# Performance work log

Measured on AMD Instinct MI355X. Metric: run time of the kernel, lower is better.

Reference implementation:

```python
import jax, jax.numpy as jnp
import numpy as np

D_MODEL = 1024
NUM_HEADS = 16
D_K = D_MODEL // NUM_HEADS
D_FF = 4096


def setup_inputs() -> dict:
    key = jax.random.key(0)
    ks = jax.random.split(key, 12)
    s = 1.0 / np.sqrt(D_MODEL)
    sf = 1.0 / np.sqrt(D_FF)
    return {
        "x": jax.random.normal(ks[0], (2, 2048, D_MODEL), dtype=jnp.float32),
        # nn.Linear weights are [out_features, in_features]
        "Wq": jax.random.uniform(ks[1], (D_MODEL, D_MODEL), jnp.float32, -s, s),
        "Wk": jax.random.uniform(ks[2], (D_MODEL, D_MODEL), jnp.float32, -s, s),
        "Wv": jax.random.uniform(ks[3], (D_MODEL, D_MODEL), jnp.float32, -s, s),
        "Wo": jax.random.uniform(ks[4], (D_MODEL, D_MODEL), jnp.float32, -s, s),
        "W1": jax.random.uniform(ks[5], (D_FF, D_MODEL), jnp.float32, -s, s),
        "W2": jax.random.uniform(ks[6], (D_MODEL, D_FF), jnp.float32, -sf, sf),
        "g1": jnp.ones((D_MODEL,), jnp.float32),
        "b1": jnp.zeros((D_MODEL,), jnp.float32),
        "g2": jnp.ones((D_MODEL,), jnp.float32),
        "b2": jnp.zeros((D_MODEL,), jnp.float32),
    }


def _layer_norm(x, gamma, beta, eps=1e-5):
    mu = jnp.mean(x, axis=-1, keepdims=True)
    var = jnp.mean((x - mu) ** 2, axis=-1, keepdims=True)
    return (x - mu) * jax.lax.rsqrt(var + eps) * gamma + beta


def reference(x, Wq, Wk, Wv, Wo, W1, W2, g1, b1, g2, b2):
    B, S, _ = x.shape
    H, Dk = NUM_HEADS, D_K
    # projections (Linear: x @ W.T), split heads -> [B, H, S, Dk]
    q = (x @ Wq.T).reshape(B, S, H, Dk).transpose(0, 2, 1, 3)
    k = (x @ Wk.T).reshape(B, S, H, Dk).transpose(0, 2, 1, 3)
    v = (x @ Wv.T).reshape(B, S, H, Dk).transpose(0, 2, 1, 3)
    scores = jnp.einsum('bhsd,bhtd->bhst', q, k) / jnp.sqrt(jnp.float32(Dk))
    attn = jax.nn.softmax(scores, axis=-1)
    out = jnp.einsum('bhst,bhtd->bhsd', attn, v)
    out = out.transpose(0, 2, 1, 3).reshape(B, S, H * Dk)
    out = out @ Wo.T
    x_after_attn = _layer_norm(x + out, g1, b1)
    ff = jax.nn.gelu(x_after_attn @ W1.T, approximate=False)
    ff_out = ff @ W2.T
    return _layer_norm(x_after_attn + ff_out, g2, b2)
```

## Files before the change

### kernel.cpp

```cpp
#include <hip/hip_runtime.h>
#include <hip/hip_bf16.h>
#include <cstdint>
#include <cstddef>

#define D_MODEL 1024
#define D_FF    4096
#define NTOK    4096
#define SEQ     2048
#define NH      16
#define DK      64
#define LDQ     3072

typedef __bf16 bf16;
typedef __bf16 bf16_8 __attribute__((ext_vector_type(8)));
typedef __bf16 bf16_4 __attribute__((ext_vector_type(4)));
typedef float  f32_4  __attribute__((ext_vector_type(4)));

__device__ __forceinline__ void async_copy16(const bf16* g, bf16* l) {
    __builtin_amdgcn_global_load_lds((const __attribute__((address_space(1))) void*)g,
                                     (__attribute__((address_space(3))) void*)l,
                                     16, 0, 0);
}

__global__ __launch_bounds__(256)
void cast_all(const float* __restrict__ x,  const float* __restrict__ Wq,
              const float* __restrict__ Wk, const float* __restrict__ Wv,
              const float* __restrict__ Wo, const float* __restrict__ W1,
              const float* __restrict__ W2,
              bf16* __restrict__ xb, bf16* __restrict__ Wqkvb,
              bf16* __restrict__ Wob, bf16* __restrict__ W1b,
              bf16* __restrict__ W2b) {
    const int blk = blockIdx.x;
    const float* s; bf16* d; int off;
    if (blk < 4096)       { s = x;  d = xb;              off = blk; }
    else if (blk < 5120)  { s = Wq; d = Wqkvb;           off = blk - 4096; }
    else if (blk < 6144)  { s = Wk; d = Wqkvb + 1048576; off = blk - 5120; }
    else if (blk < 7168)  { s = Wv; d = Wqkvb + 2097152; off = blk - 6144; }
    else if (blk < 8192)  { s = Wo; d = Wob;             off = blk - 7168; }
    else if (blk < 12288) { s = W1; d = W1b;             off = blk - 8192; }
    else                  { s = W2; d = W2b;             off = blk - 12288; }
    const int i = off * 1024 + threadIdx.x * 4;
    float4 v = *(const float4*)(s + i);
    bf16_4 o;
    o[0] = (bf16)v.x; o[1] = (bf16)v.y; o[2] = (bf16)v.z; o[3] = (bf16)v.w;
    *(bf16_4*)(d + i) = o;
}

template <int EPI>
__global__ __launch_bounds__(256, 2)
void gemm_bt(const bf16* __restrict__ A, const bf16* __restrict__ B,
             bf16* __restrict__ C0, size_t cstride, bf16* __restrict__ Vt,
             int M, int N, int ldk, int kLen) {
    __shared__ bf16 As[128 * 64];
    __shared__ bf16 Bs[128 * 64];
    const int tid  = threadIdx.x;
    const int wave = tid >> 6, lane = tid & 63;
    const int quad = lane >> 4, l15 = lane & 15;
    const int wm = wave >> 1, wn = wave & 1;
    const int bm = blockIdx.x, bn = blockIdx.y, z = blockIdx.z;

    const bf16* A0 = A + (size_t)bm * 128 * ldk + (size_t)z * kLen;
    const bf16* B0 = B + (size_t)bn * 128 * ldk + (size_t)z * kLen;

    f32_4 acc[4][4];
#pragma unroll
    for (int i = 0; i < 4; i++)
#pragma unroll
        for (int j = 0; j < 4; j++) acc[i][j] = (f32_4){0.f, 0.f, 0.f, 0.f};

    const int srow8 = lane >> 3;
    const int slog  = (lane & 7) ^ srow8;
    const int rx    = l15 & 7;

    for (int k0 = 0; k0 < kLen; k0 += 64) {
#pragma unroll
        for (int c = 0; c < 4; c++) {
            int row = c * 32 + wave * 8 + srow8;
            async_copy16(&A0[(size_t)row * ldk + k0 + slog * 8],
                         &As[(c * 32 + wave * 8) * 64]);
        }
#pragma unroll
        for (int c = 0; c < 4; c++) {
            int row = c * 32 + wave * 8 + srow8;
            async_copy16(&B0[(size_t)row * ldk + k0 + slog * 8],
                         &Bs[(c * 32 + wave * 8) * 64]);
        }
        __syncthreads();

#pragma unroll
        for (int kh = 0; kh < 2; kh++) {
            bf16_8 af[4], bfr[4];
#pragma unroll
            for (int mi = 0; mi < 4; mi++)
                af[mi] = *(const bf16_8*)&As[(wm * 64 + mi * 16 + l15) * 64 +
                                             (((kh * 4 + quad) ^ rx) * 8)];
#pragma unroll
            for (int ni = 0; ni < 4; ni++)
                bfr[ni] = *(const bf16_8*)&Bs[(wn * 64 + ni * 16 + l15) * 64 +
                                              (((kh * 4 + quad) ^ rx) * 8)];
#pragma unroll
            for (int mi = 0; mi < 4; mi++)
#pragma unroll
                for (int ni = 0; ni < 4; ni++)
                    acc[mi][ni] = __builtin_amdgcn_mfma_f32_16x16x32_bf16(
                        af[mi], bfr[ni], acc[mi][ni], 0, 0, 0);
        }
        __syncthreads();
    }

    bf16* C = C0 + (size_t)z * cstride;
    const int row0 = bm * 128 + wm * 64 + quad * 4;
    const int col0 = bn * 128 + wn * 64 + l15;

    if (EPI == 3 && bn >= 16) {
        const int bvt = bm >> 4;
#pragma unroll
        for (int mi = 0; mi < 4; mi++) {
            const int srow = (row0 + mi * 16) & 2047;
#pragma unroll
            for (int ni = 0; ni < 4; ni++) {
                const int ch = col0 + ni * 16 - 2048;
                bf16_4 w;
#pragma unroll
                for (int r = 0; r < 4; r++) w[r] = (bf16)acc[mi][ni][r];
                *(bf16_4*)&Vt[((size_t)(bvt * 1024 + ch)) * SEQ + srow] = w;
            }
        }
        return;
    }

#pragma unroll
    for (int mi = 0; mi < 4; mi++) {
#pragma unroll
        for (int ni = 0; ni < 4; ni++) {
#pragma unroll
            for (int r = 0; r < 4; r++) {
                int row = row0 + mi * 16 + r;
                int col = col0 + ni * 16;
                size_t idx = (size_t)row * N + col;
                float v = acc[mi][ni][r];
                if (EPI == 2) {
                    float g = 0.5f * v * (1.0f + erff(v * 0.70710678118654752f));
                    C[idx] = (bf16)g;
                } else {
                    C[idx] = (bf16)v;
                }
            }
        }
    }
}

__global__ __launch_bounds__(512)
void attn8(const bf16* __restrict__ QKV, const bf16* __restrict__ Vt,
           bf16* __restrict__ O) {
    __shared__ bf16 SM[2][8192];

    const int tid  = threadIdx.x;
    const int wave = tid >> 6, lane = tid & 63;
    const int quad = lane >> 4, l15 = lane & 15;
    const int qb = blockIdx.x & 15;
    const int h  = (blockIdx.x >> 4) & 15;
    const int b  = blockIdx.x >> 8;

    const bf16* Qg = QKV + (size_t)(b * SEQ) * LDQ + h * 64;
    const bf16* Kg = QKV + (size_t)(b * SEQ) * LDQ + 1024 + h * 64;
    const bf16* Vg = Vt + (size_t)(b * 1024 + h * 64) * SEQ;

    const int qrow = qb * 128 + wave * 16 + l15;
    const bf16_8 qf0 = *(const bf16_8*)&Qg[(size_t)qrow * LDQ + quad * 8];
    const bf16_8 qf1 = *(const bf16_8*)&Qg[(size_t)qrow * LDQ + 32 + quad * 8];

    const int m0 = wave * 8 + (lane >> 3);
    const int sg = lane & 7;
    const int sw = m0 & 7;
    const int xl = l15 & 7;
    const int fr = (((m0 >> 4) & 1) << 5) | ((m0 & 12) << 1) |
                   (((m0 >> 5) & 1) << 2) | (m0 & 3);

    bf16_8 one8;
#pragma unroll
    for (int i = 0; i < 8; i++) one8[i] = (bf16)1.0f;

    f32_4 lacc = (f32_4){0.f, 0.f, 0.f, 0.f};
    f32_4 o_acc[4];
#pragma unroll
    for (int d = 0; d < 4; d++) o_acc[d] = (f32_4){0.f, 0.f, 0.f, 0.f};

    async_copy16(&Kg[(size_t)fr * LDQ + ((sg ^ sw) * 8)],
                 &SM[0][wave * 512]);
    async_copy16(&Vg[(size_t)m0 * SEQ + ((sg ^ sw) * 8)],
                 &SM[0][4096 + wave * 512]);
    __syncthreads();

    for (int t = 0; t < SEQ / 64; ++t) {
        const int cur = t & 1;
        if (t + 1 < SEQ / 64) {
            const int k1 = (t + 1) * 64;
            async_copy16(&Kg[(size_t)(k1 + fr) * LDQ + ((sg ^ sw) * 8)],
                         &SM[cur ^ 1][wave * 512]);
            async_copy16(&Vg[(size_t)m0 * SEQ + k1 + ((sg ^ sw) * 8)],
                         &SM[cur ^ 1][4096 + wave * 512]);
        }

        const bf16* KsC = SM[cur];
        const bf16* VsC = SM[cur] + 4096;

        f32_4 s[4];
#pragma unroll
        for (int ni = 0; ni < 4; ni++) {
            const bf16* kp = &KsC[(ni * 16 + l15) * 64];
            bf16_8 kb0 = *(const bf16_8*)&kp[(quad ^ xl) * 8];
            bf16_8 kb1 = *(const bf16_8*)&kp[((quad + 4) ^ xl) * 8];
            f32_4 zz = (f32_4){0.f, 0.f, 0.f, 0.f};
            zz = __builtin_amdgcn_mfma_f32_16x16x32_bf16(kb0, qf0, zz, 0, 0, 0);
            s[ni] = __builtin_amdgcn_mfma_f32_16x16x32_bf16(kb1, qf1, zz, 0, 0, 0);
        }

        bf16_8 pf0, pf1;
#pragma unroll
        for (int ni = 0; ni < 4; ni++) {
#pragma unroll
            for (int r = 0; r < 4; r++) {
                float p = __expf(fmaf(s[ni][r], 0.125f, -8.0f));
                bf16 pb = (bf16)p;
                const int jx = ((ni >> 1) << 2) + r;
                if ((ni & 1) == 0) pf0[jx] = pb;
                else               pf1[jx] = pb;
            }
        }

        lacc = __builtin_amdgcn_mfma_f32_16x16x32_bf16(one8, pf0, lacc, 0, 0, 0);
        lacc = __builtin_amdgcn_mfma_f32_16x16x32_bf16(one8, pf1, lacc, 0, 0, 0);

#pragma unroll
        for (int dt = 0; dt < 4; dt++) {
            const bf16* vp = &VsC[(dt * 16 + l15) * 64];
            bf16_8 vb0 = *(const bf16_8*)&vp[(quad ^ xl) * 8];
            bf16_8 vb1 = *(const bf16_8*)&vp[((quad + 4) ^ xl) * 8];
            o_acc[dt] = __builtin_amdgcn_mfma_f32_16x16x32_bf16(vb0, pf0, o_acc[dt], 0, 0, 0);
            o_acc[dt] = __builtin_amdgcn_mfma_f32_16x16x32_bf16(vb1, pf1, o_acc[dt], 0, 0, 0);
        }

        __syncthreads();
    }

    const float rl = 1.0f / lacc[0];

    bf16* P = (bf16*)SM + wave * 1280;
#pragma unroll
    for (int dt = 0; dt < 4; dt++) {
        bf16_4 pk;
#pragma unroll
        for (int r = 0; r < 4; r++) pk[r] = (bf16)(o_acc[dt][r] * rl);
        int G = dt * 2 + (quad >> 1);
        *(bf16_4*)&P[l15 * 80 + ((G ^ xl) * 8) + ((quad & 1) * 4)] = pk;
    }
    const int q2 = lane >> 2, dc = lane & 3, x2 = q2 & 7;
    bf16_8 o0 = *(const bf16_8*)&P[q2 * 80 + (((dc * 2) ^ x2) * 8)];
    bf16_8 o1 = *(const bf16_8*)&P[q2 * 80 + (((dc * 2 + 1) ^ x2) * 8)];
    const size_t row = (size_t)b * SEQ + qb * 128 + wave * 16 + q2;
    *(bf16_8*)&O[row * D_MODEL + h * 64 + dc * 16] = o0;
    *(bf16_8*)&O[row * D_MODEL + h * 64 + dc * 16 + 8] = o1;
}

template <bool A32, bool O32>
__global__ __launch_bounds__(256)
void ln_kernel(const void* __restrict__ av, const bf16* __restrict__ p0,
               const bf16* __restrict__ p1, const bf16* __restrict__ p2,
               const bf16* __restrict__ p3,
               const float* __restrict__ gamma, const float* __restrict__ beta,
               void* __restrict__ yv) {
    const int row = blockIdx.x;
    const int tid = threadIdx.x;
    const size_t off = (size_t)row * D_MODEL;
    float v[4];
    {
        bf16_4 a0 = *(const bf16_4*)(p0 + off + tid * 4);
        bf16_4 a1 = *(const bf16_4*)(p1 + off + tid * 4);
        bf16_4 a2 = *(const bf16_4*)(p2 + off + tid * 4);
        bf16_4 a3 = *(const bf16_4*)(p3 + off + tid * 4);
        if (A32) {
            float4 xa = *(const float4*)((const float*)av + off + tid * 4);
            v[0] = xa.x; v[1] = xa.y; v[2] = xa.z; v[3] = xa.w;
        } else {
            bf16_4 xa = *(const bf16_4*)((const bf16*)av + off + tid * 4);
#pragma unroll
            for (int i = 0; i < 4; i++) v[i] = (float)xa[i];
        }
#pragma unroll
        for (int i = 0; i < 4; i++)
            v[i] += ((float)a0[i] + (float)a1[i]) + ((float)a2[i] + (float)a3[i]);
    }
    float s = v[0] + v[1] + v[2] + v[3];
    float ss = v[0] * v[0] + v[1] * v[1] + v[2] * v[2] + v[3] * v[3];
#pragma unroll
    for (int m = 1; m < 64; m <<= 1) {
        s  += __shfl_xor(s, m);
        ss += __shfl_xor(ss, m);
    }
    __shared__ float red_s[4], red_q[4];
    int wave = tid >> 6, lane = tid & 63;
    if (lane == 0) { red_s[wave] = s; red_q[wave] = ss; }
    __syncthreads();
    s  = red_s[0] + red_s[1] + red_s[2] + red_s[3];
    ss = red_q[0] + red_q[1] + red_q[2] + red_q[3];
    float mu   = s * (1.f / D_MODEL);
    float var  = ss * (1.f / D_MODEL) - mu * mu;
    float rstd = rsqrtf(var + 1e-5f);
    float4 gg = *(const float4*)(gamma + tid * 4);
    float4 be = *(const float4*)(beta + tid * 4);
    float y0 = (v[0] - mu) * rstd * gg.x + be.x;
    float y1 = (v[1] - mu) * rstd * gg.y + be.y;
    float y2 = (v[2] - mu) * rstd * gg.z + be.z;
    float y3 = (v[3] - mu) * rstd * gg.w + be.w;
    if (O32) {
        *(float4*)((float*)yv + off + tid * 4) = make_float4(y0, y1, y2, y3);
    } else {
        bf16_4 o;
        o[0] = (bf16)y0; o[1] = (bf16)y1; o[2] = (bf16)y2; o[3] = (bf16)y3;
        *(bf16_4*)((bf16*)yv + off + tid * 4) = o;
    }
}

extern "C" void kernel_launch(void* const* d_in, const int* in_sizes, int n_in,
                              void* d_out, int out_size, void* d_ws, size_t ws_size,
                              hipStream_t stream) {
    (void)in_sizes; (void)n_in; (void)out_size; (void)ws_size;
    const float* x  = (const float*)d_in[0];
    const float* Wq = (const float*)d_in[1];
    const float* Wk = (const float*)d_in[2];
    const float* Wv = (const float*)d_in[3];
    const float* Wo = (const float*)d_in[4];
    const float* W1 = (const float*)d_in[5];
    const float* W2 = (const float*)d_in[6];
    const float* g1 = (const float*)d_in[7];
    const float* b1 = (const float*)d_in[8];
    const float* g2 = (const float*)d_in[9];
    const float* b2 = (const float*)d_in[10];

    char* ws = (char*)d_ws;
    bf16*  xb    = (bf16*)(ws + 0);
    bf16*  aob   = xb;
    bf16*  ln1b  = (bf16*)(ws + 0);
    bf16*  QKVb  = (bf16*)(ws + 8388608);
    bf16*  Vtb   = (bf16*)(ws + 33554432);
    bf16*  hb    = (bf16*)(ws + 8388608);
    bf16*  Wqkvb = (bf16*)(ws + 41943040);
    bf16*  Wob   = (bf16*)(ws + 48234496);
    bf16*  W1b   = (bf16*)(ws + 50331648);
    bf16*  W2b   = (bf16*)(ws + 58720256);
    bf16*  proj0 = (bf16*)(ws + 67108864);
    const size_t PSTRIDE = (size_t)NTOK * D_MODEL;

    cast_all<<<dim3(16384), 256, 0, stream>>>(x, Wq, Wk, Wv, Wo, W1, W2,
                                              xb, Wqkvb, Wob, W1b, W2b);

    gemm_bt<3><<<dim3(NTOK / 128, 3072 / 128, 1), 256, 0, stream>>>(
        xb, Wqkvb, QKVb, 0, Vtb, NTOK, 3072, D_MODEL, D_MODEL);

    attn8<<<dim3(512), 512, 0, stream>>>(QKVb, Vtb, aob);

    gemm_bt<0><<<dim3(NTOK / 128, D_MODEL / 128, 4), 256, 0, stream>>>(
        aob, Wob, proj0, PSTRIDE, nullptr, NTOK, D_MODEL, D_MODEL, 256);
    ln_kernel<true, false><<<NTOK, 256, 0, stream>>>(
        x, proj0, proj0 + PSTRIDE, proj0 + 2 * PSTRIDE, proj0 + 3 * PSTRIDE,
        g1, b1, ln1b);

    gemm_bt<2><<<dim3(NTOK / 128, D_FF / 128, 1), 256, 0, stream>>>(
        ln1b, W1b, hb, 0, nullptr, NTOK, D_FF, D_MODEL, D_MODEL);

    gemm_bt<0><<<dim3(NTOK / 128, D_MODEL / 128, 4), 256, 0, stream>>>(
        hb, W2b, proj0, PSTRIDE, nullptr, NTOK, D_MODEL, D_FF, 1024);
    ln_kernel<false, true><<<NTOK, 256, 0, stream>>>(
        ln1b, proj0, proj0 + PSTRIDE, proj0 + 2 * PSTRIDE, proj0 + 3 * PSTRIDE,
        g2, b2, d_out);
}
```

Measured before the change: 298.2 us.

## Double attention KV tile to 128 keys and raise GEMM occupancy hint

The attention kernel now processes 128 keys per loop iteration instead of 64, with a larger double-buffered LDS tile and a new swizzle for the 128-wide V tile. This halves the number of barriers and loop iterations and gives more MFMA work per sync. The GEMM launch bounds hint is raised from 2 to 3 blocks per SU, which may force register spilling. The larger LDS use (64KB per attention block) and the higher register pressure may reduce occupancy.

```diff
diff --git a/kernel.cpp b/kernel.cpp
--- a/kernel.cpp
+++ b/kernel.cpp
@@ -47,7 +47,7 @@
 }
 
 template <int EPI>
-__global__ __launch_bounds__(256, 2)
+__global__ __launch_bounds__(256, 3)
 void gemm_bt(const bf16* __restrict__ A, const bf16* __restrict__ B,
              bf16* __restrict__ C0, size_t cstride, bf16* __restrict__ Vt,
              int M, int N, int ldk, int kLen) {
@@ -150,10 +150,10 @@
     }
 }
 
-__global__ __launch_bounds__(512)
-void attn8(const bf16* __restrict__ QKV, const bf16* __restrict__ Vt,
+__global__ __launch_bounds__(512, 4)
+void attn9(const bf16* __restrict__ QKV, const bf16* __restrict__ Vt,
            bf16* __restrict__ O) {
-    __shared__ bf16 SM[2][8192];
+    __shared__ bf16 SM[2][16384];
 
     const int tid  = threadIdx.x;
     const int wave = tid >> 6, lane = tid & 63;
@@ -172,10 +172,13 @@
 
     const int m0 = wave * 8 + (lane >> 3);
     const int sg = lane & 7;
-    const int sw = m0 & 7;
-    const int xl = l15 & 7;
+    const int swk = m0 & 7;
     const int fr = (((m0 >> 4) & 1) << 5) | ((m0 & 12) << 1) |
                    (((m0 >> 5) & 1) << 2) | (m0 & 3);
+    const int vr0 = wave * 4 + (lane >> 4);
+    const int vg  = lane & 15;
+    const int swv = vr0 & 7;
+    const int xl  = l15 & 7;
 
     bf16_8 one8;
 #pragma unroll
@@ -186,28 +189,38 @@
 #pragma unroll
     for (int d = 0; d < 4; d++) o_acc[d] = (f32_4){0.f, 0.f, 0.f, 0.f};
 
-    async_copy16(&Kg[(size_t)fr * LDQ + ((sg ^ sw) * 8)],
-                 &SM[0][wave * 512]);
-    async_copy16(&Vg[(size_t)m0 * SEQ + ((sg ^ sw) * 8)],
-                 &SM[0][4096 + wave * 512]);
+    async_copy16(&Kg[(size_t)fr * LDQ + ((sg ^ swk) * 8)],
+                 &SM[0][(wave * 8) * 64]);
+    async_copy16(&Kg[(size_t)(fr + 64) * LDQ + ((sg ^ swk) * 8)],
+                 &SM[0][(64 + wave * 8) * 64]);
+    async_copy16(&Vg[(size_t)vr0 * SEQ + ((vg ^ swv) * 8)],
+                 &SM[0][8192 + (wave * 4) * 128]);
+    async_copy16(&Vg[(size_t)(vr0 + 32) * SEQ + ((vg ^ swv) * 8)],
+                 &SM[0][8192 + (32 + wave * 4) * 128]);
     __syncthreads();
 
-    for (int t = 0; t < SEQ / 64; ++t) {
+    const int NT = SEQ / 128;
+    for (int t = 0; t < NT; ++t) {
         const int cur = t & 1;
-        if (t + 1 < SEQ / 64) {
-            const int k1 = (t + 1) * 64;
-            async_copy16(&Kg[(size_t)(k1 + fr) * LDQ + ((sg ^ sw) * 8)],
-                         &SM[cur ^ 1][wave * 512]);
-            async_copy16(&Vg[(size_t)m0 * SEQ + k1 + ((sg ^ sw) * 8)],
-                         &SM[cur ^ 1][4096 + wave * 512]);
+        if (t + 1 < NT) {
+            const int k1 = (t + 1) * 128;
+            bf16* kd = SM[cur ^ 1];
+            async_copy16(&Kg[(size_t)(k1 + fr) * LDQ + ((sg ^ swk) * 8)],
+                         kd + (wave * 8) * 64);
+            async_copy16(&Kg[(size_t)(k1 + fr + 64) * LDQ + ((sg ^ swk) * 8)],
+                         kd + (64 + wave * 8) * 64);
+            async_copy16(&Vg[(size_t)vr0 * SEQ + k1 + ((vg ^ swv) * 8)],
+                         kd + 8192 + (wave * 4) * 128);
+            async_copy16(&Vg[(size_t)(vr0 + 32) * SEQ + k1 + ((vg ^ swv) * 8)],
+                         kd + 8192 + (32 + wave * 4) * 128);
         }
 
         const bf16* KsC = SM[cur];
-        const bf16* VsC = SM[cur] + 4096;
-
-        f32_4 s[4];
-#pragma unroll
-        for (int ni = 0; ni < 4; ni++) {
+        const bf16* VsC = SM[cur] + 8192;
+
+        f32_4 s[8];
+#pragma unroll
+        for (int ni = 0; ni < 8; ni++) {
             const bf16* kp = &KsC[(ni * 16 + l15) * 64];
             bf16_8 kb0 = *(const bf16_8*)&kp[(quad ^ xl) * 8];
             bf16_8 kb1 = *(const bf16_8*)&kp[((quad + 4) ^ xl) * 8];
@@ -216,29 +229,31 @@
             s[ni] = __builtin_amdgcn_mfma_f32_16x16x32_bf16(kb1, qf1, zz, 0, 0, 0);
         }
 
-        bf16_8 pf0, pf1;
-#pragma unroll
-        for (int ni = 0; ni < 4; ni++) {
+        bf16_8 pf[4];
+#pragma unroll
+        for (int ni = 0; ni < 8; ni++) {
 #pragma unroll
             for (int r = 0; r < 4; r++) {
                 float p = __expf(fmaf(s[ni][r], 0.125f, -8.0f));
                 bf16 pb = (bf16)p;
-                const int jx = ((ni >> 1) << 2) + r;
-                if ((ni & 1) == 0) pf0[jx] = pb;
-                else               pf1[jx] = pb;
+                const int jx = (((ni >> 1) & 1) << 2) + r;
+                pf[(ni & 1) + ((ni >> 2) << 1)][jx] = pb;
             }
         }
 
-        lacc = __builtin_amdgcn_mfma_f32_16x16x32_bf16(one8, pf0, lacc, 0, 0, 0);
-        lacc = __builtin_amdgcn_mfma_f32_16x16x32_bf16(one8, pf1, lacc, 0, 0, 0);
+#pragma unroll
+        for (int ks = 0; ks < 4; ks++)
+            lacc = __builtin_amdgcn_mfma_f32_16x16x32_bf16(one8, pf[ks], lacc, 0, 0, 0);
 
 #pragma unroll
         for (int dt = 0; dt < 4; dt++) {
-            const bf16* vp = &VsC[(dt * 16 + l15) * 64];
-            bf16_8 vb0 = *(const bf16_8*)&vp[(quad ^ xl) * 8];
-            bf16_8 vb1 = *(const bf16_8*)&vp[((quad + 4) ^ xl) * 8];
-            o_acc[dt] = __builtin_amdgcn_mfma_f32_16x16x32_bf16(vb0, pf0, o_acc[dt], 0, 0, 0);
-            o_acc[dt] = __builtin_amdgcn_mfma_f32_16x16x32_bf16(vb1, pf1, o_acc[dt], 0, 0, 0);
+            const bf16* vp = &VsC[(dt * 16 + l15) * 128];
+#pragma unroll
+            for (int ks = 0; ks < 4; ks++) {
+                bf16_8 vb = *(const bf16_8*)&vp[(((ks * 4 + quad) ^ xl)) * 8];
+                o_acc[dt] = __builtin_amdgcn_mfma_f32_16x16x32_bf16(
+                    vb, pf[ks], o_acc[dt], 0, 0, 0);
+            }
         }
 
         __syncthreads();
@@ -358,7 +373,7 @@
     gemm_bt<3><<<dim3(NTOK / 128, 3072 / 128, 1), 256, 0, stream>>>(
         xb, Wqkvb, QKVb, 0, Vtb, NTOK, 3072, D_MODEL, D_MODEL);
 
-    attn8<<<dim3(512), 512, 0, stream>>>(QKVb, Vtb, aob);
+    attn9<<<dim3(512), 512, 0, stream>>>(QKVb, Vtb, aob);
 
     gemm_bt<0><<<dim3(NTOK / 128, D_MODEL / 128, 4), 256, 0, stream>>>(
         aob, Wob, proj0, PSTRIDE, nullptr, NTOK, D_MODEL, D_MODEL, 256);
```

Result: slower. 309.6 us (+3.8%).
